# Kernel tuning notes

Hardware: AMD Instinct MI355X
Metric: run time of the kernel (lower is better)

Reference implementation:

```python
import jax, jax.numpy as jnp
import numpy as np

# Model config (matches init_kwargs)
B, T, D = 2, 2048, 2048
H, KH, F = 16, 4, 8192
HD = D // H            # 128
G = H // KH            # q heads per kv head = 4
EPS = 1e-5


def _ln(x, g, b):
    m = jnp.mean(x, axis=-1, keepdims=True)
    v = jnp.mean((x - m) ** 2, axis=-1, keepdims=True)
    return (x - m) * jax.lax.rsqrt(v + EPS) * g + b


def setup_inputs() -> dict:
    key = jax.random.key(0)
    ks = jax.random.split(key, 8)

    def xav(k, shape):
        lim = (6.0 / (shape[0] + shape[1])) ** 0.5
        return jax.random.uniform(k, shape, jnp.float32, -lim, lim)

    x = jax.random.normal(ks[0], (B, T, D), jnp.float32)
    mask = jnp.tril(jnp.ones((1, 1, T, T), jnp.int32))  # causal
    # Linear weights stored as [in, out] (transpose of torch nn.Linear)
    return {
        "x": x,
        "mask": mask,
        "Wq": xav(ks[1], (D, H * HD)), "bq": jnp.zeros((H * HD,), jnp.float32),
        "Wk": xav(ks[2], (D, KH * HD)), "bk": jnp.zeros((KH * HD,), jnp.float32),
        "Wv": xav(ks[3], (D, KH * HD)), "bv": jnp.zeros((KH * HD,), jnp.float32),
        "Wo": xav(ks[4], (H * HD, D)), "bo": jnp.zeros((D,), jnp.float32),
        "ln1_g": jnp.ones((D,), jnp.float32), "ln1_b": jnp.zeros((D,), jnp.float32),
        "ln2_g": jnp.ones((D,), jnp.float32), "ln2_b": jnp.zeros((D,), jnp.float32),
        "fln_g": jnp.ones((D,), jnp.float32), "fln_b": jnp.zeros((D,), jnp.float32),
        "W1": xav(ks[5], (D, F)), "b1": jnp.zeros((F,), jnp.float32),
        "W2": xav(ks[6], (D, F)), "b2": jnp.zeros((F,), jnp.float32),
        "W3": xav(ks[7], (F, D)), "b3": jnp.zeros((D,), jnp.float32),
    }


def reference(x, mask, Wq, bq, Wk, bk, Wv, bv, Wo, bo,
              ln1_g, ln1_b, ln2_g, ln2_b, fln_g, fln_b,
              W1, b1, W2, b2, W3, b3):
    scale = 1.0 / np.sqrt(HD)
    # --- attention block (pre-LN + residual) ---
    h = _ln(x, ln1_g, ln1_b)
    q = (h @ Wq + bq).reshape(B, T, KH, G, HD)   # q head k*G+g uses kv head k
    k = (h @ Wk + bk).reshape(B, T, KH, HD)
    v = (h @ Wv + bv).reshape(B, T, KH, HD)
    # GQA scores without repeat_interleave: broadcast kv head across group g
    scores = jnp.einsum('btkgd,bskd->bkgts', q, k) * scale  # [B,KH,G,T,T]
    scores = jnp.clip(scores, -100.0, 100.0)
    scores = jnp.where(mask[:, :, None] == 0, -jnp.inf, scores)
    attn = jax.nn.softmax(scores, axis=-1)
    ctx = jnp.einsum('bkgts,bskd->btkgd', attn, v).reshape(B, T, H * HD)
    x = x + (ctx @ Wo + bo)  # dropout is identity in eval
    # --- ln2 then SwiGLU FFN (which has its own internal LN and residual
    # around the *post-ln2* activation, faithful to original) ---
    x = _ln(x, ln2_g, ln2_b)
    r = x
    h2 = _ln(x, fln_g, fln_b)
    g_pre = h2 @ W1 + b1
    gate = g_pre * jax.nn.sigmoid(jnp.clip(g_pre, -10.0, 10.0))
    hidden = h2 @ W2 + b2
    return r + ((gate * hidden) @ W3 + b3)
```

## Files before the change

kernel.cpp:

```cpp
#include <hip/hip_runtime.h>
#include <math.h>
#include <stdint.h>

typedef __bf16 bf16_t;
typedef __bf16 bf16x4 __attribute__((ext_vector_type(4)));
typedef __bf16 bf16x8 __attribute__((ext_vector_type(8)));
typedef float  f32x4  __attribute__((ext_vector_type(4)));

#define D_MODEL 2048
#define T_SEQ   2048
#define BATCH   2
#define NROWS   (BATCH*T_SEQ)
#define NHEAD   16
#define HDIM    128
#define KVH     4
#define KVD     (KVH*HDIM)
#define FDIM    8192
#define QKVN    3072

__device__ __forceinline__ bf16x8 mk8(bf16x4 lo, bf16x4 hi) {
  union { bf16x4 h[2]; bf16x8 v; } u;
  u.h[0] = lo; u.h[1] = hi; return u.v;
}

__device__ __forceinline__ void gl16(const bf16_t* g, bf16_t* l) {
  __builtin_amdgcn_global_load_lds(
      (const uint32_t __attribute__((address_space(1)))*)g,
      (uint32_t __attribute__((address_space(3)))*)l, 16, 0, 0);
}

__global__ __launch_bounds__(256)
void transpose_w(const float* __restrict__ in, bf16_t* __restrict__ outT, int K, int N)
{
  __shared__ __align__(16) bf16_t t[64][72];
  const int tid = threadIdx.x;
  const int k0 = blockIdx.y * 64, n0 = blockIdx.x * 64;
  const int tr = tid >> 4, tc = (tid & 15) * 4;
#pragma unroll
  for (int i = 0; i < 4; ++i) {
    f32x4 v = *(const f32x4*)(in + (size_t)(k0 + tr + 16 * i) * N + n0 + tc);
#pragma unroll
    for (int e = 0; e < 4; ++e) t[tr + 16 * i][tc + e] = (bf16_t)v[e];
  }
  __syncthreads();
#pragma unroll
  for (int s = 0; s < 2; ++s) {
    const int c = s * 256 + tid;
    const int n = c >> 3, c8 = (c & 7) * 8;
    bf16x8 o;
#pragma unroll
    for (int e = 0; e < 8; ++e) o[e] = t[c8 + e][n];
    *(bf16x8*)(outT + (size_t)(n0 + n) * K + k0 + c8) = o;
  }
}

__global__ __launch_bounds__(256)
void concat_bias(const float* __restrict__ a, const float* __restrict__ b,
                 const float* __restrict__ c, float* __restrict__ dst)
{
  const int i = blockIdx.x * 256 + threadIdx.x;
  if (i >= QKVN) return;
  dst[i] = (i < 2048) ? a[i] : (i < 2560) ? b[i - 2048] : c[i - 2560];
}

template<typename TI>
__global__ __launch_bounds__(256)
void ln_kernel(const TI* __restrict__ x, const float* __restrict__ g,
               const float* __restrict__ b, bf16_t* __restrict__ out)
{
  const int row = blockIdx.x;
  const int tid = threadIdx.x;
  const TI* xr = x + (size_t)row * D_MODEL;
  float vals[8];
  if constexpr (sizeof(TI) == 4) {
    f32x4 v0 = *(const f32x4*)(xr + tid * 8);
    f32x4 v1 = *(const f32x4*)(xr + tid * 8 + 4);
#pragma unroll
    for (int e = 0; e < 4; ++e) { vals[e] = v0[e]; vals[4 + e] = v1[e]; }
  } else {
    bf16x8 v = *(const bf16x8*)(xr + tid * 8);
#pragma unroll
    for (int e = 0; e < 8; ++e) vals[e] = (float)v[e];
  }
  float s = 0.f, s2 = 0.f;
#pragma unroll
  for (int e = 0; e < 8; ++e) { s += vals[e]; s2 += vals[e] * vals[e]; }
#pragma unroll
  for (int off = 1; off < 64; off <<= 1) { s += __shfl_xor(s, off); s2 += __shfl_xor(s2, off); }
  __shared__ float red[8];
  const int wid = tid >> 6, lane = tid & 63;
  if (lane == 0) { red[wid] = s; red[4 + wid] = s2; }
  __syncthreads();
  s  = red[0] + red[1] + red[2] + red[3];
  s2 = red[4] + red[5] + red[6] + red[7];
  const float mean = s * (1.f / D_MODEL);
  const float var  = s2 * (1.f / D_MODEL) - mean * mean;
  const float rstd = rsqrtf(var + 1e-5f);
  f32x4 g0 = *(const f32x4*)(g + tid * 8), g1 = *(const f32x4*)(g + tid * 8 + 4);
  f32x4 b0 = *(const f32x4*)(b + tid * 8), b1 = *(const f32x4*)(b + tid * 8 + 4);
  bf16x8 o;
#pragma unroll
  for (int e = 0; e < 4; ++e) {
    o[e]     = (bf16_t)((vals[e]     - mean) * rstd * g0[e] + b0[e]);
    o[4 + e] = (bf16_t)((vals[4 + e] - mean) * rstd * g1[e] + b1[e]);
  }
  *(bf16x8*)(out + (size_t)row * D_MODEL + tid * 8) = o;
}

__global__ __launch_bounds__(256)
void ln2_fused(const bf16_t* __restrict__ x, const float* __restrict__ g2,
               const float* __restrict__ b2, const float* __restrict__ gf,
               const float* __restrict__ bf_, bf16_t* __restrict__ rout,
               bf16_t* __restrict__ hout)
{
  const int row = blockIdx.x;
  const int tid = threadIdx.x;
  const int wid = tid >> 6, lane = tid & 63;
  __shared__ float red[8];
  const bf16_t* xr = x + (size_t)row * D_MODEL;
  bf16x8 v = *(const bf16x8*)(xr + tid * 8);
  float vals[8]; float s = 0.f, s2 = 0.f;
#pragma unroll
  for (int e = 0; e < 8; ++e) { vals[e] = (float)v[e]; s += vals[e]; s2 += vals[e] * vals[e]; }
#pragma unroll
  for (int off = 1; off < 64; off <<= 1) { s += __shfl_xor(s, off); s2 += __shfl_xor(s2, off); }
  if (lane == 0) { red[wid] = s; red[4 + wid] = s2; }
  __syncthreads();
  s  = red[0] + red[1] + red[2] + red[3];
  s2 = red[4] + red[5] + red[6] + red[7];
  float mean = s * (1.f / D_MODEL);
  float var  = s2 * (1.f / D_MODEL) - mean * mean;
  float rstd = rsqrtf(var + 1e-5f);
  f32x4 ga0 = *(const f32x4*)(g2 + tid * 8), ga1 = *(const f32x4*)(g2 + tid * 8 + 4);
  f32x4 ba0 = *(const f32x4*)(b2 + tid * 8), ba1 = *(const f32x4*)(b2 + tid * 8 + 4);
  float y[8];
#pragma unroll
  for (int e = 0; e < 4; ++e) {
    y[e]     = (vals[e]     - mean) * rstd * ga0[e] + ba0[e];
    y[4 + e] = (vals[4 + e] - mean) * rstd * ga1[e] + ba1[e];
  }
  bf16x8 o1;
#pragma unroll
  for (int e = 0; e < 8; ++e) o1[e] = (bf16_t)y[e];
  *(bf16x8*)(rout + (size_t)row * D_MODEL + tid * 8) = o1;
  s = 0.f; s2 = 0.f;
#pragma unroll
  for (int e = 0; e < 8; ++e) { s += y[e]; s2 += y[e] * y[e]; }
#pragma unroll
  for (int off = 1; off < 64; off <<= 1) { s += __shfl_xor(s, off); s2 += __shfl_xor(s2, off); }
  __syncthreads();
  if (lane == 0) { red[wid] = s; red[4 + wid] = s2; }
  __syncthreads();
  s  = red[0] + red[1] + red[2] + red[3];
  s2 = red[4] + red[5] + red[6] + red[7];
  mean = s * (1.f / D_MODEL);
  var  = s2 * (1.f / D_MODEL) - mean * mean;
  rstd = rsqrtf(var + 1e-5f);
  f32x4 gb0 = *(const f32x4*)(gf + tid * 8), gb1 = *(const f32x4*)(gf + tid * 8 + 4);
  f32x4 bb0 = *(const f32x4*)(bf_ + tid * 8), bb1 = *(const f32x4*)(bf_ + tid * 8 + 4);
  bf16x8 o2;
#pragma unroll
  for (int e = 0; e < 4; ++e) {
    o2[e]     = (bf16_t)((y[e]     - mean) * rstd * gb0[e] + bb0[e]);
    o2[4 + e] = (bf16_t)((y[4 + e] - mean) * rstd * gb1[e] + bb1[e]);
  }
  *(bf16x8*)(hout + (size_t)row * D_MODEL + tid * 8) = o2;
}

enum { EPI_NONE = 0, EPI_RES = 1, EPI_SILU = 2, EPI_MUL = 3 };

__device__ __forceinline__ void xcd_swz(int BMv, int BNv, int& m0, int& n0) {
  const int nbx = gridDim.x, nwg = nbx * gridDim.y;
  int flat = blockIdx.y * nbx + blockIdx.x;
  flat = (flat & 7) * (nwg >> 3) + (flat >> 3);
  m0 = (flat / nbx) * BMv; n0 = (flat % nbx) * BNv;
}

template<int EPI, int BM_T, typename TE, typename TO>
__global__ __launch_bounds__(512, 2)
void gemm8p(const bf16_t* __restrict__ A, const bf16_t* __restrict__ Bt,
            const float* __restrict__ bias, const TE* __restrict__ extra,
            TO* __restrict__ out, int M, int N, int K)
{
  constexpr int ALs = BM_T / 128;
  constexpr int RF  = BM_T / 32;
  __shared__ __align__(16) bf16_t As[2][2][BM_T * 32];
  __shared__ __align__(16) bf16_t Bs[2][2][256 * 32];
  const int tid = threadIdx.x, lane = tid & 63, wid = tid >> 6;
  const int wr = wid >> 2, wc = wid & 3;
  const int l16 = lane & 15, lq = lane >> 4;
  int m0, n0; xcd_swz(BM_T, 256, m0, n0);

  const bf16_t* aP[ALs]; int aL[ALs];
#pragma unroll
  for (int s = 0; s < ALs; ++s) {
    const int c = s * 512 + tid;
    const int row = c >> 2, pos = c & 3;
    aP[s] = A + (size_t)(m0 + row) * K + (pos ^ ((row >> 1) & 3)) * 8;
    aL[s] = (s * 512 + wid * 64) * 8;
  }
  const bf16_t* bP[2]; int bL[2];
#pragma unroll
  for (int s = 0; s < 2; ++s) {
    const int c = s * 512 + tid;
    const int row = c >> 2, pos = c & 3;
    bP[s] = Bt + (size_t)(n0 + row) * K + (pos ^ ((row >> 1) & 3)) * 8;
    bL[s] = (s * 512 + wid * 64) * 8;
  }

  int offA[RF];
#pragma unroll
  for (int i = 0; i < RF; ++i) {
    const int r = wr * (BM_T / 2) + i * 16 + l16;
    offA[i] = r * 32 + ((lq ^ ((r >> 1) & 3)) * 8);
  }
  int offB[4];
#pragma unroll
  for (int jj = 0; jj < 4; ++jj) {
    const int r = wc * 64 + jj * 16 + l16;
    offB[jj] = r * 32 + ((lq ^ ((r >> 1) & 3)) * 8);
  }

  f32x4 acc[RF][4];
#pragma unroll
  for (int i = 0; i < RF; ++i)
#pragma unroll
    for (int j = 0; j < 4; ++j) acc[i][j] = (f32x4){0.f, 0.f, 0.f, 0.f};

  auto SA = [&](int t, int bb, int kh) {
#pragma unroll
    for (int s = 0; s < ALs; ++s) gl16(aP[s] + t * 64 + kh * 32, &As[bb][kh][aL[s]]);
  };
  auto SB = [&](int t, int bb, int kh) {
#pragma unroll
    for (int s = 0; s < 2; ++s) gl16(bP[s] + t * 64 + kh * 32, &Bs[bb][kh][bL[s]]);
  };
#define BAR_()  __builtin_amdgcn_s_barrier()
#define LGKM_() do { asm volatile("s_waitcnt lgkmcnt(0)" ::: "memory"); \
                     __builtin_amdgcn_sched_barrier(0); } while (0)

  const int nt = K >> 6;
  SA(0, 0, 0); SB(0, 0, 0); SA(0, 0, 1); SB(0, 0, 1);
  if (nt > 1) { SA(1, 1, 0); SB(1, 1, 0); SA(1, 1, 1); }
  if (nt > 2) {
    if constexpr (ALs == 2) asm volatile("s_waitcnt vmcnt(6)" ::: "memory");
    else                    asm volatile("s_waitcnt vmcnt(4)" ::: "memory");
  } else {
    asm volatile("s_waitcnt vmcnt(0)" ::: "memory");
  }
  BAR_();

  for (int t = 0; t < nt; ++t) {
    const int b = t & 1, ob = b ^ 1;
    const bool s1 = (t + 1 < nt), s2 = (t + 2 < nt);
    bf16x8 af[RF], bf0, bf1;
#pragma unroll
    for (int i = 0; i < RF; ++i) af[i] = *(const bf16x8*)(&As[b][0][offA[i]]);
    bf0 = *(const bf16x8*)(&Bs[b][0][offB[0]]);
    bf1 = *(const bf16x8*)(&Bs[b][0][offB[1]]);
    if (s1) SB(t + 1, ob, 1);
    BAR_(); LGKM_();
    __builtin_amdgcn_s_setprio(1);
#pragma unroll
    for (int i = 0; i < RF; ++i) {
      acc[i][0] = __builtin_amdgcn_mfma_f32_16x16x32_bf16(af[i], bf0, acc[i][0], 0, 0, 0);
      acc[i][1] = __builtin_amdgcn_mfma_f32_16x16x32_bf16(af[i], bf1, acc[i][1], 0, 0, 0);
    }
    __builtin_amdgcn_s_setprio(0);
    BAR_();
    bf0 = *(const bf16x8*)(&Bs[b][0][offB[2]]);
    bf1 = *(const bf16x8*)(&Bs[b][0][offB[3]]);
    if (s2) SA(t + 2, b, 0);
    BAR_(); LGKM_();
    __builtin_amdgcn_s_setprio(1);
#pragma unroll
    for (int i = 0; i < RF; ++i) {
      acc[i][2] = __builtin_amdgcn_mfma_f32_16x16x32_bf16(af[i], bf0, acc[i][2], 0, 0, 0);
      acc[i][3] = __builtin_amdgcn_mfma_f32_16x16x32_bf16(af[i], bf1, acc[i][3], 0, 0, 0);
    }
    __builtin_amdgcn_s_setprio(0);
    BAR_();
#pragma unroll
    for (int i = 0; i < RF; ++i) af[i] = *(const bf16x8*)(&As[b][1][offA[i]]);
    bf0 = *(const bf16x8*)(&Bs[b][1][offB[0]]);
    bf1 = *(const bf16x8*)(&Bs[b][1][offB[1]]);
    if (s2) SB(t + 2, b, 0);
    BAR_(); LGKM_();
    __builtin_amdgcn_s_setprio(1);
#pragma unroll
    for (int i = 0; i < RF; ++i) {
      acc[i][0] = __builtin_amdgcn_mfma_f32_16x16x32_bf16(af[i], bf0, acc[i][0], 0, 0, 0);
      acc[i][1] = __builtin_amdgcn_mfma_f32_16x16x32_bf16(af[i], bf1, acc[i][1], 0, 0, 0);
    }
    __builtin_amdgcn_s_setprio(0);
    BAR_();
    bf0 = *(const bf16x8*)(&Bs[b][1][offB[2]]);
    bf1 = *(const bf16x8*)(&Bs[b][1][offB[3]]);
    if (s2) SA(t + 2, b, 1);
    BAR_(); LGKM_();
    __builtin_amdgcn_s_setprio(1);
#pragma unroll
    for (int i = 0; i < RF; ++i) {
      acc[i][2] = __builtin_amdgcn_mfma_f32_16x16x32_bf16(af[i], bf0, acc[i][2], 0, 0, 0);
      acc[i][3] = __builtin_amdgcn_mfma_f32_16x16x32_bf16(af[i], bf1, acc[i][3], 0, 0, 0);
    }
    __builtin_amdgcn_s_setprio(0);
    if (t < nt - 2) {
      if constexpr (ALs == 2) asm volatile("s_waitcnt vmcnt(6)" ::: "memory");
      else                    asm volatile("s_waitcnt vmcnt(4)" ::: "memory");
    } else {
      asm volatile("s_waitcnt vmcnt(0)" ::: "memory");
    }
    BAR_();
  }

  if constexpr (sizeof(TO) == 2) {
    float* sc = (float*)(&As[0][0][0]) + (size_t)wid * (16 * 72);
    const int rr = lane >> 3, cc8 = (lane & 7) * 8;
#pragma unroll
    for (int i = 0; i < RF; ++i) {
      const int row0 = m0 + wr * (BM_T / 2) + i * 16;
#pragma unroll
      for (int j = 0; j < 4; ++j) {
        const float bb = bias[n0 + wc * 64 + j * 16 + l16];
#pragma unroll
        for (int e = 0; e < 4; ++e) {
          float vv = acc[i][j][e] + bb;
          if (EPI == EPI_SILU) { float c2 = fminf(fmaxf(vv, -10.f), 10.f); vv = vv / (1.f + __expf(-c2)); }
          sc[(lq * 4 + e) * 72 + j * 16 + l16] = vv;
        }
      }
      asm volatile("s_waitcnt lgkmcnt(0)" ::: "memory");
      __builtin_amdgcn_sched_barrier(0);
#pragma unroll
      for (int q = 0; q < 2; ++q) {
        const int row = row0 + rr + q * 8;
        const size_t base = (size_t)row * N + n0 + wc * 64 + cc8;
        f32x4 a0 = *(const f32x4*)(sc + (rr + q * 8) * 72 + cc8);
        f32x4 a1 = *(const f32x4*)(sc + (rr + q * 8) * 72 + cc8 + 4);
        bf16x8 o;
        if constexpr (EPI == EPI_RES) {
          if constexpr (sizeof(TE) == 4) {
            f32x4 x0 = *(const f32x4*)((const float*)extra + base);
            f32x4 x1 = *(const f32x4*)((const float*)extra + base + 4);
#pragma unroll
            for (int e = 0; e < 4; ++e) { o[e] = (bf16_t)(a0[e] + x0[e]); o[4 + e] = (bf16_t)(a1[e] + x1[e]); }
          } else {
            bf16x8 x8 = *(const bf16x8*)((const bf16_t*)extra + base);
#pragma unroll
            for (int e = 0; e < 4; ++e) { o[e] = (bf16_t)(a0[e] + (float)x8[e]); o[4 + e] = (bf16_t)(a1[e] + (float)x8[4 + e]); }
          }
        } else if constexpr (EPI == EPI_MUL) {
          bf16x8 x8 = *(const bf16x8*)((const bf16_t*)extra + base);
#pragma unroll
          for (int e = 0; e < 4; ++e) { o[e] = (bf16_t)(a0[e] * (float)x8[e]); o[4 + e] = (bf16_t)(a1[e] * (float)x8[4 + e]); }
        } else {
#pragma unroll
          for (int e = 0; e < 4; ++e) { o[e] = (bf16_t)a0[e]; o[4 + e] = (bf16_t)a1[e]; }
        }
        *(bf16x8*)((bf16_t*)out + base) = o;
      }
      asm volatile("s_waitcnt lgkmcnt(0)" ::: "memory");
      __builtin_amdgcn_sched_barrier(0);
    }
  } else {
#pragma unroll
    for (int j = 0; j < 4; ++j) {
      const int col = n0 + wc * 64 + j * 16 + l16;
      const float bb = bias[col];
#pragma unroll
      for (int i = 0; i < RF; ++i) {
        const int row0 = m0 + wr * (BM_T / 2) + i * 16 + lq * 4;
#pragma unroll
        for (int e = 0; e < 4; ++e) {
          const size_t idx = (size_t)(row0 + e) * N + col;
          float vv = acc[i][j][e] + bb;
          if (EPI == EPI_RES)       vv += (float)extra[idx];
          else if (EPI == EPI_SILU) { float c2 = fminf(fmaxf(vv, -10.f), 10.f); vv = vv / (1.f + __expf(-c2)); }
          else if (EPI == EPI_MUL)  vv *= (float)extra[idx];
          out[idx] = (TO)vv;
        }
      }
    }
  }
#undef BAR_
#undef LGKM_
}

template<int EPI, typename TE, typename TO>
__global__ __launch_bounds__(256, 4)
void gemm3b(const bf16_t* __restrict__ A, const bf16_t* __restrict__ Bt,
            const float* __restrict__ bias, const TE* __restrict__ extra,
            TO* __restrict__ out, int M, int N, int K)
{
  __shared__ __align__(16) bf16_t As[3][128 * 32];
  __shared__ __align__(16) bf16_t Bs[3][128 * 32];
  const int tid = threadIdx.x, lane = tid & 63, wid = tid >> 6;
  const int wr = wid >> 1, wc = wid & 1;
  const int l16 = lane & 15, lq = lane >> 4;
  int m0, n0; xcd_swz(128, 128, m0, n0);

  const bf16_t* aP[2]; const bf16_t* bP[2]; int sL[2];
#pragma unroll
  for (int s = 0; s < 2; ++s) {
    const int c = s * 256 + tid;
    const int row = c >> 2, pos = c & 3;
    const int g = pos ^ ((row >> 1) & 3);
    aP[s] = A  + (size_t)(m0 + row) * K + g * 8;
    bP[s] = Bt + (size_t)(n0 + row) * K + g * 8;
    sL[s] = (s * 256 + wid * 64) * 8;
  }

  int offA[4], offB[4];
#pragma unroll
  for (int i = 0; i < 4; ++i) {
    const int r = wr * 64 + i * 16 + l16;
    offA[i] = r * 32 + ((lq ^ ((r >> 1) & 3)) * 8);
  }
#pragma unroll
  for (int j = 0; j < 4; ++j) {
    const int r = wc * 64 + j * 16 + l16;
    offB[j] = r * 32 + ((lq ^ ((r >> 1) & 3)) * 8);
  }

  f32x4 acc[4][4];
#pragma unroll
  for (int i = 0; i < 4; ++i)
#pragma unroll
    for (int j = 0; j < 4; ++j) acc[i][j] = (f32x4){0.f, 0.f, 0.f, 0.f};

  auto STAGE = [&](int t, int b) {
    gl16(aP[0] + t * 32, &As[b][sL[0]]);
    gl16(aP[1] + t * 32, &As[b][sL[1]]);
    gl16(bP[0] + t * 32, &Bs[b][sL[0]]);
    gl16(bP[1] + t * 32, &Bs[b][sL[1]]);
  };

  const int nt = K >> 5;
  STAGE(0, 0);
  STAGE(1, 1);
  if (nt > 1) asm volatile("s_waitcnt vmcnt(4)" ::: "memory");
  else        asm volatile("s_waitcnt vmcnt(0)" ::: "memory");
  __builtin_amdgcn_s_barrier();

  int b = 0;
  for (int t = 0; t < nt; ++t) {
    bf16x8 af[4], bfr[4];
#pragma unroll
    for (int i = 0; i < 4; ++i) af[i]  = *(const bf16x8*)(&As[b][offA[i]]);
#pragma unroll
    for (int j = 0; j < 4; ++j) bfr[j] = *(const bf16x8*)(&Bs[b][offB[j]]);
    if (t + 2 < nt) {
      STAGE(t + 2, (b + 2) % 3);
      asm volatile("s_waitcnt vmcnt(4)" ::: "memory");
    } else {
      asm volatile("s_waitcnt vmcnt(0)" ::: "memory");
    }
    __builtin_amdgcn_s_barrier();
    asm volatile("s_waitcnt lgkmcnt(0)" ::: "memory");
    __builtin_amdgcn_sched_barrier(0);
    __builtin_amdgcn_s_setprio(1);
#pragma unroll
    for (int i = 0; i < 4; ++i)
#pragma unroll
      for (int j = 0; j < 4; ++j)
        acc[i][j] = __builtin_amdgcn_mfma_f32_16x16x32_bf16(af[i], bfr[j], acc[i][j], 0, 0, 0);
    __builtin_amdgcn_s_setprio(0);
    __builtin_amdgcn_s_barrier();
    b = (b + 1) % 3;
  }

  if constexpr (sizeof(TO) == 2) {
    float* sc = (float*)(&As[0][0]) + (size_t)wid * (16 * 72);
    const int rr = lane >> 3, cc8 = (lane & 7) * 8;
#pragma unroll
    for (int i = 0; i < 4; ++i) {
      const int row0 = m0 + wr * 64 + i * 16;
#pragma unroll
      for (int j = 0; j < 4; ++j) {
        const float bb = bias[n0 + wc * 64 + j * 16 + l16];
#pragma unroll
        for (int e = 0; e < 4; ++e) {
          float vv = acc[i][j][e] + bb;
          if (EPI == EPI_SILU) { float c2 = fminf(fmaxf(vv, -10.f), 10.f); vv = vv / (1.f + __expf(-c2)); }
          sc[(lq * 4 + e) * 72 + j * 16 + l16] = vv;
        }
      }
      asm volatile("s_waitcnt lgkmcnt(0)" ::: "memory");
      __builtin_amdgcn_sched_barrier(0);
#pragma unroll
      for (int q = 0; q < 2; ++q) {
        const int row = row0 + rr + q * 8;
        const size_t base = (size_t)row * N + n0 + wc * 64 + cc8;
        f32x4 a0 = *(const f32x4*)(sc + (rr + q * 8) * 72 + cc8);
        f32x4 a1 = *(const f32x4*)(sc + (rr + q * 8) * 72 + cc8 + 4);
        bf16x8 o;
        if constexpr (EPI == EPI_RES) {
          if constexpr (sizeof(TE) == 4) {
            f32x4 x0 = *(const f32x4*)((const float*)extra + base);
            f32x4 x1 = *(const f32x4*)((const float*)extra + base + 4);
#pragma unroll
            for (int e = 0; e < 4; ++e) { o[e] = (bf16_t)(a0[e] + x0[e]); o[4 + e] = (bf16_t)(a1[e] + x1[e]); }
          } else {
            bf16x8 x8 = *(const bf16x8*)((const bf16_t*)extra + base);
#pragma unroll
            for (int e = 0; e < 4; ++e) { o[e] = (bf16_t)(a0[e] + (float)x8[e]); o[4 + e] = (bf16_t)(a1[e] + (float)x8[4 + e]); }
          }
        } else if constexpr (EPI == EPI_MUL) {
          bf16x8 x8 = *(const bf16x8*)((const bf16_t*)extra + base);
#pragma unroll
          for (int e = 0; e < 4; ++e) { o[e] = (bf16_t)(a0[e] * (float)x8[e]); o[4 + e] = (bf16_t)(a1[e] * (float)x8[4 + e]); }
        } else {
#pragma unroll
          for (int e = 0; e < 4; ++e) { o[e] = (bf16_t)a0[e]; o[4 + e] = (bf16_t)a1[e]; }
        }
        *(bf16x8*)((bf16_t*)out + base) = o;
      }
      asm volatile("s_waitcnt lgkmcnt(0)" ::: "memory");
      __builtin_amdgcn_sched_barrier(0);
    }
  } else {
#pragma unroll
    for (int j = 0; j < 4; ++j) {
      const int col = n0 + wc * 64 + j * 16 + l16;
      const float bb = bias[col];
#pragma unroll
      for (int i = 0; i < 4; ++i) {
        const int row0 = m0 + wr * 64 + i * 16 + lq * 4;
#pragma unroll
        for (int e = 0; e < 4; ++e) {
          const size_t idx = (size_t)(row0 + e) * N + col;
          float vv = acc[i][j][e] + bb;
          if (EPI == EPI_RES)       vv += (float)extra[idx];
          else if (EPI == EPI_SILU) { float c2 = fminf(fmaxf(vv, -10.f), 10.f); vv = vv / (1.f + __expf(-c2)); }
          else if (EPI == EPI_MUL)  vv *= (float)extra[idx];
          out[idx] = (TO)vv;
        }
      }
    }
  }
}

template<int EPI, typename TE, typename TO>
__global__ __launch_bounds__(256)
void gemm_kernel(const bf16_t* __restrict__ A, const float* __restrict__ W,
                 const float* __restrict__ bias, const TE* __restrict__ extra,
                 TO* __restrict__ out, int M, int N, int K)
{
  __shared__ bf16_t As[128][40];
  __shared__ bf16_t Bs[128][40];
  const int tid  = threadIdx.x;
  const int lane = tid & 63, wid = tid >> 6;
  const int wr = wid >> 1, wc = wid & 1;
  const int l16 = lane & 15, lq = lane >> 4;
  const int m0 = blockIdx.y * 128, n0 = blockIdx.x * 128;

  f32x4 acc[4][4];
#pragma unroll
  for (int i = 0; i < 4; ++i)
#pragma unroll
    for (int j = 0; j < 4; ++j) acc[i][j] = (f32x4){0.f, 0.f, 0.f, 0.f};

  const int ar = tid >> 1, ah = tid & 1;
  const int kk = tid & 31, cc = tid >> 5;

  for (int k0 = 0; k0 < K; k0 += 32) {
    const bf16_t* asrc = A + (size_t)(m0 + ar) * K + k0 + ah * 16;
    *(bf16x8*)(&As[ar][ah * 16])     = *(const bf16x8*)(asrc);
    *(bf16x8*)(&As[ar][ah * 16 + 8]) = *(const bf16x8*)(asrc + 8);
    const float* wsrc = W + (size_t)(k0 + kk) * N + n0;
#pragma unroll
    for (int it = 0; it < 2; ++it) {
      const int c = cc * 8 + it * 64;
      f32x4 wa = *(const f32x4*)(wsrc + c);
      f32x4 wb = *(const f32x4*)(wsrc + c + 4);
#pragma unroll
      for (int e = 0; e < 4; ++e) {
        Bs[c + e][kk]     = (bf16_t)wa[e];
        Bs[c + 4 + e][kk] = (bf16_t)wb[e];
      }
    }
    __syncthreads();
    bf16x8 af[4], bfr[4];
#pragma unroll
    for (int i = 0; i < 4; ++i) {
      const bf16_t* p = &As[wr * 64 + i * 16 + l16][lq * 4];
      af[i] = mk8(*(const bf16x4*)p, *(const bf16x4*)(p + 16));
    }
#pragma unroll
    for (int j = 0; j < 4; ++j) {
      const bf16_t* p = &Bs[wc * 64 + j * 16 + l16][lq * 4];
      bfr[j] = mk8(*(const bf16x4*)p, *(const bf16x4*)(p + 16));
    }
#pragma unroll
    for (int i = 0; i < 4; ++i)
#pragma unroll
      for (int j = 0; j < 4; ++j)
        acc[i][j] = __builtin_amdgcn_mfma_f32_16x16x32_bf16(af[i], bfr[j], acc[i][j], 0, 0, 0);
    __syncthreads();
  }

#pragma unroll
  for (int j = 0; j < 4; ++j) {
    const int col = n0 + wc * 64 + j * 16 + l16;
    const float bb = bias[col];
#pragma unroll
    for (int i = 0; i < 4; ++i) {
      const int row0 = m0 + wr * 64 + i * 16 + lq * 4;
#pragma unroll
      for (int e = 0; e < 4; ++e) {
        const size_t idx = (size_t)(row0 + e) * N + col;
        float vv = acc[i][j][e] + bb;
        if (EPI == EPI_RES)       vv += (float)extra[idx];
        else if (EPI == EPI_SILU) { float c2 = fminf(fmaxf(vv, -10.f), 10.f); vv = vv / (1.f + __expf(-c2)); }
        else if (EPI == EPI_MUL)  vv *= (float)extra[idx];
        out[idx] = (TO)vv;
      }
    }
  }
}

__global__ __launch_bounds__(256)
void attn_kernel(const bf16_t* __restrict__ q, const bf16_t* __restrict__ k,
                 const bf16_t* __restrict__ v, bf16_t* __restrict__ ctx,
                 int q_ld, int kv_ld)
{
  __shared__ __align__(16) bf16_t Ks[64 * 128];
  __shared__ __align__(16) bf16_t Vt[128][72];

  const int tid = threadIdx.x, lane = tid & 63, wid = tid >> 6;
  const int l16 = lane & 15, lq = lane >> 4;
  const int bh = blockIdx.y;
  const int b = bh >> 4, h = bh & 15;
  const int kh = h >> 2;
  const float scale = 0.08838834764831845f;

  for (int pass = 0; pass < 2; ++pass) {
    const int qt = pass ? blockIdx.x : (31 - blockIdx.x);
    const int qbase = qt * 64;
    const int qrow = qbase + wid * 16 + l16;

    const bf16_t* qp = q + (size_t)(b * T_SEQ + qrow) * q_ld + h * HDIM;
    bf16x8 bq[4];
#pragma unroll
    for (int s = 0; s < 4; ++s) bq[s] = *(const bf16x8*)(qp + s * 32 + lq * 8);

    float m_r = -1e30f, l_r = 0.f;
    f32x4 acc_o[8];
#pragma unroll
    for (int jh = 0; jh < 8; ++jh) acc_o[jh] = (f32x4){0.f, 0.f, 0.f, 0.f};

    const int ntiles = qt + 1;
    for (int t = 0; t < ntiles; ++t) {
      const int kb = t * 64;
      __syncthreads();
#pragma unroll
      for (int it = 0; it < 4; ++it) {
        const int c = it * 256 + tid;
        const int kvr = c >> 4, pos = c & 15;
        const int src = pos ^ (kvr & 7);
        gl16(k + (size_t)(b * T_SEQ + kb + kvr) * kv_ld + kh * HDIM + src * 8,
             Ks + (size_t)(it * 256 + wid * 64) * 8);
      }
#pragma unroll
      for (int it = 0; it < 4; ++it) {
        const int c = tid + it * 256;
        const int r = c & 63, voff = (c >> 6) * 8;
        bf16x8 vv = *(const bf16x8*)(v + (size_t)(b * T_SEQ + kb + r) * kv_ld + kh * HDIM + voff);
#pragma unroll
        for (int e = 0; e < 8; ++e) Vt[voff + e][r] = vv[e];
      }
      __syncthreads();

      f32x4 sf[4];
#pragma unroll
      for (int j = 0; j < 4; ++j) {
        sf[j] = (f32x4){0.f, 0.f, 0.f, 0.f};
        const int kvr = j * 16 + l16;
#pragma unroll
        for (int s = 0; s < 4; ++s) {
          bf16x8 ak = *(const bf16x8*)(Ks + kvr * 128 + (((s * 4 + lq) ^ (kvr & 7)) * 8));
          sf[j] = __builtin_amdgcn_mfma_f32_16x16x32_bf16(ak, bq[s], sf[j], 0, 0, 0);
        }
      }

      float p[4][4];
      float tmax = -1e30f;
#pragma unroll
      for (int j = 0; j < 4; ++j)
#pragma unroll
        for (int e = 0; e < 4; ++e) {
          const int kvc = kb + j * 16 + lq * 4 + e;
          float sv = sf[j][e] * scale;
          sv = fminf(fmaxf(sv, -100.f), 100.f);
          if (kvc > qrow) sv = -1e30f;
          p[j][e] = sv;
          tmax = fmaxf(tmax, sv);
        }
      tmax = fmaxf(tmax, __shfl_xor(tmax, 16));
      tmax = fmaxf(tmax, __shfl_xor(tmax, 32));
      const float mnew = fmaxf(m_r, tmax);
      const float resc = __expf(m_r - mnew);
      m_r = mnew;
      float rsum = 0.f;
#pragma unroll
      for (int j = 0; j < 4; ++j)
#pragma unroll
        for (int e = 0; e < 4; ++e) {
          p[j][e] = __expf(p[j][e] - m_r);
          rsum += p[j][e];
        }
      rsum += __shfl_xor(rsum, 16);
      rsum += __shfl_xor(rsum, 32);
      l_r = l_r * resc + rsum;

      float resc4[4];
#pragma unroll
      for (int e = 0; e < 4; ++e) resc4[e] = __shfl(resc, lq * 4 + e);
#pragma unroll
      for (int jh = 0; jh < 8; ++jh)
#pragma unroll
        for (int e = 0; e < 4; ++e) acc_o[jh][e] *= resc4[e];

      bf16x8 pa[2];
#pragma unroll
      for (int sk = 0; sk < 2; ++sk) {
        bf16x4 lo, hi;
#pragma unroll
        for (int e = 0; e < 4; ++e) { lo[e] = (bf16_t)p[2 * sk][e]; hi[e] = (bf16_t)p[2 * sk + 1][e]; }
        pa[sk] = mk8(lo, hi);
      }
#pragma unroll
      for (int jh = 0; jh < 8; ++jh) {
#pragma unroll
        for (int sk = 0; sk < 2; ++sk) {
          const bf16_t* pV = &Vt[jh * 16 + l16][sk * 32 + lq * 4];
          bf16x8 bv2 = mk8(*(const bf16x4*)pV, *(const bf16x4*)(pV + 16));
          acc_o[jh] = __builtin_amdgcn_mfma_f32_16x16x32_bf16(pa[sk], bv2, acc_o[jh], 0, 0, 0);
        }
      }
    }

    float l4[4];
#pragma unroll
    for (int e = 0; e < 4; ++e) l4[e] = __shfl(l_r, lq * 4 + e);
    bf16_t* op = ctx + (size_t)(b * T_SEQ + qbase + wid * 16) * D_MODEL + h * HDIM;
#pragma unroll
    for (int jh = 0; jh < 8; ++jh)
#pragma unroll
      for (int e = 0; e < 4; ++e)
        op[(size_t)(lq * 4 + e) * D_MODEL + jh * 16 + l16] = (bf16_t)(acc_o[jh][e] / l4[e]);
  }
}

extern "C" void kernel_launch(void* const* d_in, const int* in_sizes, int n_in,
                              void* d_out, int out_size, void* d_ws, size_t ws_size,
                              hipStream_t stream)
{
  const float* x   = (const float*)d_in[0];
  const float* Wq  = (const float*)d_in[2];
  const float* bq  = (const float*)d_in[3];
  const float* Wk  = (const float*)d_in[4];
  const float* bk  = (const float*)d_in[5];
  const float* Wv  = (const float*)d_in[6];
  const float* bv  = (const float*)d_in[7];
  const float* Wo  = (const float*)d_in[8];
  const float* bo  = (const float*)d_in[9];
  const float* g1  = (const float*)d_in[10];
  const float* b1n = (const float*)d_in[11];
  const float* g2  = (const float*)d_in[12];
  const float* b2n = (const float*)d_in[13];
  const float* gf  = (const float*)d_in[14];
  const float* bfn = (const float*)d_in[15];
  const float* W1  = (const float*)d_in[16];
  const float* bb1 = (const float*)d_in[17];
  const float* W2  = (const float*)d_in[18];
  const float* bb2 = (const float*)d_in[19];
  const float* W3  = (const float*)d_in[20];
  const float* bb3 = (const float*)d_in[21];
  float* out = (float*)d_out;

  char* ws = (char*)d_ws;
  size_t off = 0;
  auto alloc = [&](size_t bytes) -> void* {
    void* p = ws + off; off += (bytes + 255) & ~(size_t)255; return p;
  };
  const dim3 blk(256);

  bf16_t* Wt_qkv = (bf16_t*)alloc((size_t)QKVN * D_MODEL * 2);
  bf16_t* Wt_o   = (bf16_t*)alloc((size_t)D_MODEL * D_MODEL * 2);
  bf16_t* Wt1    = (bf16_t*)alloc((size_t)FDIM * D_MODEL * 2);
  bf16_t* Wt2    = (bf16_t*)alloc((size_t)FDIM * D_MODEL * 2);
  bf16_t* Wt3    = (bf16_t*)alloc((size_t)D_MODEL * FDIM * 2);
  float*  bqkv   = (float*)alloc((size_t)QKVN * 4);
  bf16_t* hbuf   = (bf16_t*)alloc((size_t)NROWS * D_MODEL * 2);
  bf16_t* qkvbuf = (bf16_t*)alloc((size_t)NROWS * QKVN * 2);
  bf16_t* rbuf   = (bf16_t*)alloc((size_t)NROWS * D_MODEL * 2);
  bf16_t* h2buf  = (bf16_t*)alloc((size_t)NROWS * D_MODEL * 2);
  const size_t core = off;

  if (core <= ws_size) {
    size_t avail = ws_size - core;
    int chunk = (int)((avail / ((size_t)FDIM * 2)) & ~(size_t)255);
    bf16_t* gbuf;
    if (chunk >= 256) { gbuf = (bf16_t*)(ws + core); if (chunk > NROWS) chunk = NROWS; }
    else              { gbuf = qkvbuf; chunk = 1536; }
    bf16_t* x1buf = qkvbuf;

    transpose_w<<<dim3(32, 32),  blk, 0, stream>>>(Wq, Wt_qkv, D_MODEL, 2048);
    transpose_w<<<dim3(8, 32),   blk, 0, stream>>>(Wk, Wt_qkv + (size_t)2048 * D_MODEL, D_MODEL, 512);
    transpose_w<<<dim3(8, 32),   blk, 0, stream>>>(Wv, Wt_qkv + (size_t)2560 * D_MODEL, D_MODEL, 512);
    transpose_w<<<dim3(32, 32),  blk, 0, stream>>>(Wo, Wt_o, D_MODEL, D_MODEL);
    transpose_w<<<dim3(128, 32), blk, 0, stream>>>(W1, Wt1, D_MODEL, FDIM);
    transpose_w<<<dim3(128, 32), blk, 0, stream>>>(W2, Wt2, D_MODEL, FDIM);
    transpose_w<<<dim3(32, 128), blk, 0, stream>>>(W3, Wt3, FDIM, D_MODEL);
    concat_bias<<<12, blk, 0, stream>>>(bq, bk, bv, bqkv);

    ln_kernel<float><<<NROWS, blk, 0, stream>>>(x, g1, b1n, hbuf);
    gemm8p<EPI_NONE, 256, bf16_t, bf16_t><<<dim3(QKVN / 256, NROWS / 256), 512, 0, stream>>>(
        hbuf, Wt_qkv, bqkv, nullptr, qkvbuf, NROWS, QKVN, D_MODEL);
    attn_kernel<<<dim3(16, 32), blk, 0, stream>>>(
        qkvbuf, qkvbuf + 2048, qkvbuf + 2560, hbuf, QKVN, QKVN);
    gemm3b<EPI_RES, float, bf16_t><<<dim3(D_MODEL / 128, NROWS / 128), blk, 0, stream>>>(
        hbuf, Wt_o, bo, x, x1buf, NROWS, D_MODEL, D_MODEL);
    ln2_fused<<<NROWS, blk, 0, stream>>>(x1buf, g2, b2n, gf, bfn, rbuf, h2buf);

    for (int r0 = 0; r0 < NROWS; r0 += chunk) {
      const int rows = (NROWS - r0 < chunk) ? (NROWS - r0) : chunk;
      gemm8p<EPI_SILU, 256, bf16_t, bf16_t><<<dim3(FDIM / 256, rows / 256), 512, 0, stream>>>(
          h2buf + (size_t)r0 * D_MODEL, Wt1, bb1, nullptr, gbuf, rows, FDIM, D_MODEL);
      gemm8p<EPI_MUL, 256, bf16_t, bf16_t><<<dim3(FDIM / 256, rows / 256), 512, 0, stream>>>(
          h2buf + (size_t)r0 * D_MODEL, Wt2, bb2, gbuf, gbuf, rows, FDIM, D_MODEL);
      gemm3b<EPI_RES, bf16_t, float><<<dim3(D_MODEL / 128, rows / 128), blk, 0, stream>>>(
          gbuf, Wt3, bb3, rbuf + (size_t)r0 * D_MODEL, out + (size_t)r0 * D_MODEL, rows, D_MODEL, FDIM);
    }
    return;
  }

  off = 0;
  const size_t DBYTES = (size_t)NROWS * D_MODEL * 2;
  bf16_t* fhbuf  = (bf16_t*)alloc(DBYTES);
  bf16_t* fqbuf  = (bf16_t*)alloc(DBYTES);
  bf16_t* fkbuf  = (bf16_t*)alloc((size_t)NROWS * KVD * 2);
  bf16_t* fvbuf  = (bf16_t*)alloc((size_t)NROWS * KVD * 2);
  bf16_t* frbuf  = (bf16_t*)alloc(DBYTES);
  bf16_t* fh2buf = (bf16_t*)alloc(DBYTES);
  const size_t base = off;
  size_t avail = (ws_size > base) ? (ws_size - base) : 0;
  int chunk = (int)((avail / ((size_t)FDIM * 2)) & ~(size_t)127);
  bf16_t* gbuf;
  if (chunk >= 128) { gbuf = (bf16_t*)(ws + base); if (chunk > NROWS) chunk = NROWS; }
  else              { gbuf = fqbuf; chunk = 1024; }

  ln_kernel<float><<<NROWS, blk, 0, stream>>>(x, g1, b1n, fhbuf);
  gemm_kernel<EPI_NONE, bf16_t, bf16_t><<<dim3(16, 32), blk, 0, stream>>>(fhbuf, Wq, bq, nullptr, fqbuf, NROWS, 2048, 2048);
  gemm_kernel<EPI_NONE, bf16_t, bf16_t><<<dim3(4, 32),  blk, 0, stream>>>(fhbuf, Wk, bk, nullptr, fkbuf, NROWS, 512, 2048);
  gemm_kernel<EPI_NONE, bf16_t, bf16_t><<<dim3(4, 32),  blk, 0, stream>>>(fhbuf, Wv, bv, nullptr, fvbuf, NROWS, 512, 2048);
  attn_kernel<<<dim3(16, 32), blk, 0, stream>>>(fqbuf, fkbuf, fvbuf, fhbuf, 2048, 512);
  gemm_kernel<EPI_RES, float, bf16_t><<<dim3(16, 32), blk, 0, stream>>>(fhbuf, Wo, bo, x, fqbuf, NROWS, 2048, 2048);
  ln_kernel<bf16_t><<<NROWS, blk, 0, stream>>>(fqbuf, g2, b2n, frbuf);
  ln_kernel<bf16_t><<<NROWS, blk, 0, stream>>>(frbuf, gf, bfn, fh2buf);
  for (int r0 = 0; r0 < NROWS; r0 += chunk) {
    const int rows = (NROWS - r0 < chunk) ? (NROWS - r0) : chunk;
    gemm_kernel<EPI_SILU, bf16_t, bf16_t><<<dim3(64, rows / 128), blk, 0, stream>>>(
        fh2buf + (size_t)r0 * D_MODEL, W1, bb1, nullptr, gbuf, rows, FDIM, 2048);
    gemm_kernel<EPI_MUL, bf16_t, bf16_t><<<dim3(64, rows / 128), blk, 0, stream>>>(
        fh2buf + (size_t)r0 * D_MODEL, W2, bb2, gbuf, gbuf, rows, FDIM, 2048);
    gemm_kernel<EPI_RES, bf16_t, float><<<dim3(16, rows / 128), blk, 0, stream>>>(
        gbuf, W3, bb3, frbuf + (size_t)r0 * D_MODEL, out + (size_t)r0 * D_MODEL, rows, 2048, FDIM);
  }
}
```

Measured before the change: 776.3 us.

## Double-buffer K tiles and register-prefetch V in attention; use gemm3b for QKV

The attention kernel now keeps two K tiles in shared memory and loads the next K tile (async) and the next V tile (into registers) while the current tile is being computed. This replaces the two per-tile __syncthreads with explicit waitcnt and barriers, so global load latency can overlap with the MFMA work. Separately, the QKV projection switches from the 256-tile gemm8p to the 128-tile gemm3b kernel, which gives more blocks. The costs are extra shared memory and registers, and the synchronization is fragile: the gl16 K loads may not be covered by lgkmcnt alone.

```diff
diff --git a/kernel.cpp b/kernel.cpp
--- a/kernel.cpp
+++ b/kernel.cpp
@@ -625,7 +625,7 @@
                  const bf16_t* __restrict__ v, bf16_t* __restrict__ ctx,
                  int q_ld, int kv_ld)
 {
-  __shared__ __align__(16) bf16_t Ks[64 * 128];
+  __shared__ __align__(16) bf16_t Ks[2][64 * 128];
   __shared__ __align__(16) bf16_t Vt[128][72];
 
   const int tid = threadIdx.x, lane = tid & 63, wid = tid >> 6;
@@ -635,6 +635,8 @@
   const int kh = h >> 2;
   const float scale = 0.08838834764831845f;
 
+  const int vr = tid & 63, vo = (tid >> 6) * 8;
+
   for (int pass = 0; pass < 2; ++pass) {
     const int qt = pass ? blockIdx.x : (31 - blockIdx.x);
     const int qbase = qt * 64;
@@ -651,26 +653,43 @@
     for (int jh = 0; jh < 8; ++jh) acc_o[jh] = (f32x4){0.f, 0.f, 0.f, 0.f};
 
     const int ntiles = qt + 1;
+
+    bf16x8 vregs[4];
+#pragma unroll
+    for (int it = 0; it < 4; ++it) {
+      const int c = it * 256 + tid;
+      const int kvr = c >> 4, pos = c & 15;
+      gl16(k + (size_t)(b * T_SEQ + kvr) * kv_ld + kh * HDIM + (pos ^ (kvr & 7)) * 8,
+           &Ks[0][(it * 256 + wid * 64) * 8]);
+    }
+#pragma unroll
+    for (int it = 0; it < 4; ++it)
+      vregs[it] = *(const bf16x8*)(v + (size_t)(b * T_SEQ + vr) * kv_ld + kh * HDIM + vo + it * 32);
+
+    int cur = 0;
     for (int t = 0; t < ntiles; ++t) {
       const int kb = t * 64;
-      __syncthreads();
 #pragma unroll
       for (int it = 0; it < 4; ++it) {
-        const int c = it * 256 + tid;
-        const int kvr = c >> 4, pos = c & 15;
-        const int src = pos ^ (kvr & 7);
-        gl16(k + (size_t)(b * T_SEQ + kb + kvr) * kv_ld + kh * HDIM + src * 8,
-             Ks + (size_t)(it * 256 + wid * 64) * 8);
-      }
-#pragma unroll
-      for (int it = 0; it < 4; ++it) {
-        const int c = tid + it * 256;
-        const int r = c & 63, voff = (c >> 6) * 8;
-        bf16x8 vv = *(const bf16x8*)(v + (size_t)(b * T_SEQ + kb + r) * kv_ld + kh * HDIM + voff);
-#pragma unroll
-        for (int e = 0; e < 8; ++e) Vt[voff + e][r] = vv[e];
-      }
-      __syncthreads();
+#pragma unroll
+        for (int e = 0; e < 8; ++e) Vt[vo + it * 32 + e][vr] = vregs[it][e];
+      }
+      if (t + 1 < ntiles) {
+        const int kb2 = kb + 64;
+#pragma unroll
+        for (int it = 0; it < 4; ++it) {
+          const int c = it * 256 + tid;
+          const int kvr = c >> 4, pos = c & 15;
+          gl16(k + (size_t)(b * T_SEQ + kb2 + kvr) * kv_ld + kh * HDIM + (pos ^ (kvr & 7)) * 8,
+               &Ks[cur ^ 1][(it * 256 + wid * 64) * 8]);
+        }
+#pragma unroll
+        for (int it = 0; it < 4; ++it)
+          vregs[it] = *(const bf16x8*)(v + (size_t)(b * T_SEQ + kb2 + vr) * kv_ld + kh * HDIM + vo + it * 32);
+      }
+      asm volatile("s_waitcnt lgkmcnt(0)" ::: "memory");
+      __builtin_amdgcn_s_barrier();
+      __builtin_amdgcn_sched_barrier(0);
 
       f32x4 sf[4];
 #pragma unroll
@@ -679,7 +698,7 @@
         const int kvr = j * 16 + l16;
 #pragma unroll
         for (int s = 0; s < 4; ++s) {
-          bf16x8 ak = *(const bf16x8*)(Ks + kvr * 128 + (((s * 4 + lq) ^ (kvr & 7)) * 8));
+          bf16x8 ak = *(const bf16x8*)(&Ks[cur][kvr * 128 + (((s * 4 + lq) ^ (kvr & 7)) * 8)]);
           sf[j] = __builtin_amdgcn_mfma_f32_16x16x32_bf16(ak, bq[s], sf[j], 0, 0, 0);
         }
       }
@@ -739,6 +758,8 @@
           acc_o[jh] = __builtin_amdgcn_mfma_f32_16x16x32_bf16(pa[sk], bv2, acc_o[jh], 0, 0, 0);
         }
       }
+      __builtin_amdgcn_s_barrier();
+      cur ^= 1;
     }
 
     float l4[4];
@@ -817,7 +838,7 @@
     concat_bias<<<12, blk, 0, stream>>>(bq, bk, bv, bqkv);
 
     ln_kernel<float><<<NROWS, blk, 0, stream>>>(x, g1, b1n, hbuf);
-    gemm8p<EPI_NONE, 256, bf16_t, bf16_t><<<dim3(QKVN / 256, NROWS / 256), 512, 0, stream>>>(
+    gemm3b<EPI_NONE, bf16_t, bf16_t><<<dim3(QKVN / 128, NROWS / 128), blk, 0, stream>>>(
         hbuf, Wt_qkv, bqkv, nullptr, qkvbuf, NROWS, QKVN, D_MODEL);
     attn_kernel<<<dim3(16, 32), blk, 0, stream>>>(
         qkvbuf, qkvbuf + 2048, qkvbuf + 2560, hbuf, QKVN, QKVN);
```

New measurement: 755.0 us. 1.03x faster.
